# Optimization experiments

Hardware: AMD Instinct MI355X
Metric: run time of the kernel (lower is better)

## Reference

```python
import jax, jax.numpy as jnp
import numpy as np

N_NODES = 100000


def _gcn_conv(x, w, b, edge_index, n):
    # Linear transform
    x = x @ w + b
    # Add self loops
    loops = jnp.tile(jnp.arange(n, dtype=edge_index.dtype), (2, 1))
    ei = jnp.concatenate([edge_index, loops], axis=1)
    src, tgt = ei[0], ei[1]
    # Degree of source nodes (every node has a self loop -> deg >= 1)
    deg = jax.ops.segment_sum(jnp.ones(src.shape, x.dtype), src, num_segments=n)
    dinv = deg ** -0.5
    norm = dinv[src] * dinv[tgt]  # [E+N]
    # Gather-scale-scatter: out[t] += norm_e * x[s]
    msgs = norm[:, None] * x[src]  # [E+N, out_ch]
    return jax.ops.segment_sum(msgs, tgt, num_segments=n)


def setup_inputs() -> dict:
    key = jax.random.key(0)
    ks = jax.random.split(key, 6)
    n, f_in, hid, n_cls, e = N_NODES, 512, 16, 40, 3200000
    x = jax.random.normal(ks[0], (n, f_in), dtype=jnp.float32)
    edge_index = jax.random.randint(ks[1], (2, e), 0, n, dtype=jnp.int64)
    w1 = jax.random.normal(ks[2], (f_in, hid), dtype=jnp.float32) * (1.0 / np.sqrt(f_in))
    b1 = jax.random.normal(ks[3], (hid,), dtype=jnp.float32) * 0.01
    w2 = jax.random.normal(ks[4], (hid, n_cls), dtype=jnp.float32) * (1.0 / np.sqrt(hid))
    b2 = jax.random.normal(ks[5], (n_cls,), dtype=jnp.float32) * 0.01
    return {"x": x, "edge_index": edge_index, "w1": w1, "b1": b1, "w2": w2, "b2": b2}


def reference(x, edge_index, w1, b1, w2, b2):
    n = x.shape[0]
    h = _gcn_conv(x, w1, b1, edge_index, n)
    h = jax.nn.relu(h)
    # dropout is identity in eval mode (F.dropout with training=False)
    h = _gcn_conv(h, w2, b2, edge_index, n)
    return jax.nn.log_softmax(h, axis=1)
```

## Files before the change

### kernel.cpp

```cpp
#include <hip/hip_runtime.h>
#include <hip/hip_fp16.h>
#include <cstdint>

#define FIN 512
#define HID 16
#define NCLS 40
#define SHIFT 8
#define NBCAP 512
#define NBLK 512
#define BR 64
#define KC 32

typedef int   iv4 __attribute__((ext_vector_type(4)));
typedef float fv4 __attribute__((ext_vector_type(4)));


__global__ void count_kernel(const int* __restrict__ ei, int E, int nb,
                             int* __restrict__ hist_src_g, int* __restrict__ hist_tgt_g) {
    __shared__ int hs[NBCAP], ht[NBCAP];
    for (int j = threadIdx.x; j < NBCAP; j += 256) { hs[j] = 0; ht[j] = 0; }
    __syncthreads();
    if ((E & 3) == 0) {
        const iv4* s4 = (const iv4*)ei;
        const iv4* t4 = (const iv4*)(ei + E);
        int E4 = E >> 2;
        for (int i = blockIdx.x * 256 + threadIdx.x; i < E4; i += NBLK * 256) {
            iv4 s = __builtin_nontemporal_load(&s4[i]);
            iv4 t = __builtin_nontemporal_load(&t4[i]);
            atomicAdd(&hs[s.x >> SHIFT], 1); atomicAdd(&hs[s.y >> SHIFT], 1);
            atomicAdd(&hs[s.z >> SHIFT], 1); atomicAdd(&hs[s.w >> SHIFT], 1);
            atomicAdd(&ht[t.x >> SHIFT], 1); atomicAdd(&ht[t.y >> SHIFT], 1);
            atomicAdd(&ht[t.z >> SHIFT], 1); atomicAdd(&ht[t.w >> SHIFT], 1);
        }
    } else {
        for (int i = blockIdx.x * 256 + threadIdx.x; i < E; i += NBLK * 256) {
            atomicAdd(&hs[ei[i] >> SHIFT], 1);
            atomicAdd(&ht[ei[E + i] >> SHIFT], 1);
        }
    }
    __syncthreads();
    int base = blockIdx.x * NBCAP;
    for (int j = threadIdx.x; j < NBCAP; j += 256) {
        hist_src_g[base + j] = hs[j];
        hist_tgt_g[base + j] = ht[j];
    }
}


__global__ void colscan_kernel(int* __restrict__ hist_src_g, int* __restrict__ hist_tgt_g,
                               int* __restrict__ btot) {
    __shared__ int tmp[NBLK];
    int b = blockIdx.x;
    int* h = blockIdx.y ? hist_tgt_g : hist_src_g;
    int t = threadIdx.x;
    int v = h[t * NBCAP + b];
    tmp[t] = v;
    __syncthreads();
    for (int off = 1; off < NBLK; off <<= 1) {
        int a = (t >= off) ? tmp[t - off] : 0;
        __syncthreads();
        tmp[t] += a;
        __syncthreads();
    }
    h[t * NBCAP + b] = tmp[t] - v;
    if (t == NBLK - 1) btot[blockIdx.y * NBCAP + b] = tmp[NBLK - 1];
}


__global__ void bucketscan_kernel(const int* __restrict__ btot, int nb,
                                  int* __restrict__ src_base, int* __restrict__ tgt_base,
                                  int* __restrict__ row_ptr, int N, int E) {
    __shared__ int tmp[512];
    int t = threadIdx.x;
    int v = (t < nb) ? btot[t] : 0;
    tmp[t] = v;
    __syncthreads();
    for (int off = 1; off < 512; off <<= 1) {
        int a = (t >= off) ? tmp[t - off] : 0;
        __syncthreads();
        tmp[t] += a;
        __syncthreads();
    }
    if (t < nb) src_base[t] = tmp[t] - v;
    __syncthreads();
    int v2 = (t < nb) ? btot[NBCAP + t] : 0;
    tmp[t] = v2;
    __syncthreads();
    for (int off = 1; off < 512; off <<= 1) {
        int a = (t >= off) ? tmp[t - off] : 0;
        __syncthreads();
        tmp[t] += a;
        __syncthreads();
    }
    if (t < nb) tgt_base[t] = tmp[t] - v2;
    if (t == 0) { src_base[nb] = E; tgt_base[nb] = E; row_ptr[N] = E; }
}


__global__ void scatter_kernel(const int* __restrict__ ei, int E, int nb,
                               const int* __restrict__ hist_src_g,
                               const int* __restrict__ hist_tgt_g,
                               const int* __restrict__ src_base,
                               const int* __restrict__ tgt_base,
                               unsigned char* __restrict__ tmp_src,
                               unsigned int* __restrict__ tmp_tgt) {
    __shared__ int cs[NBCAP], ct[NBCAP];
    int blk = blockIdx.x;
    for (int j = threadIdx.x; j < nb; j += 256) {
        cs[j] = src_base[j] + hist_src_g[blk * NBCAP + j];
        ct[j] = tgt_base[j] + hist_tgt_g[blk * NBCAP + j];
    }
    __syncthreads();
    if ((E & 3) == 0) {
        const iv4* s4 = (const iv4*)ei;
        const iv4* t4 = (const iv4*)(ei + E);
        int E4 = E >> 2;
        for (int i = blk * 256 + threadIdx.x; i < E4; i += NBLK * 256) {
            iv4 s = __builtin_nontemporal_load(&s4[i]);
            iv4 t = __builtin_nontemporal_load(&t4[i]);
            int p;
            p = atomicAdd(&cs[s.x >> SHIFT], 1); tmp_src[p] = (unsigned char)(s.x & 255);
            p = atomicAdd(&cs[s.y >> SHIFT], 1); tmp_src[p] = (unsigned char)(s.y & 255);
            p = atomicAdd(&cs[s.z >> SHIFT], 1); tmp_src[p] = (unsigned char)(s.z & 255);
            p = atomicAdd(&cs[s.w >> SHIFT], 1); tmp_src[p] = (unsigned char)(s.w & 255);
            p = atomicAdd(&ct[t.x >> SHIFT], 1); tmp_tgt[p] = ((unsigned int)(t.x & 255) << 17) | (unsigned int)s.x;
            p = atomicAdd(&ct[t.y >> SHIFT], 1); tmp_tgt[p] = ((unsigned int)(t.y & 255) << 17) | (unsigned int)s.y;
            p = atomicAdd(&ct[t.z >> SHIFT], 1); tmp_tgt[p] = ((unsigned int)(t.z & 255) << 17) | (unsigned int)s.z;
            p = atomicAdd(&ct[t.w >> SHIFT], 1); tmp_tgt[p] = ((unsigned int)(t.w & 255) << 17) | (unsigned int)s.w;
        }
    } else {
        for (int i = blk * 256 + threadIdx.x; i < E; i += NBLK * 256) {
            int s = ei[i], tg = ei[E + i];
            int ps = atomicAdd(&cs[s >> SHIFT], 1);
            tmp_src[ps] = (unsigned char)(s & 255);
            int pt = atomicAdd(&ct[tg >> SHIFT], 1);
            tmp_tgt[pt] = ((unsigned int)(tg & 255) << 17) | (unsigned int)s;
        }
    }
}


__global__ void fine_kernel(const unsigned char* __restrict__ tmp_src,
                            const int* __restrict__ src_base,
                            const unsigned int* __restrict__ tmp_tgt,
                            const int* __restrict__ tgt_base,
                            float* __restrict__ dinv, int* __restrict__ row_ptr,
                            int* __restrict__ edges, int N) {
    __shared__ int hist[256];
    __shared__ int scan[256];
    int b = blockIdx.x;
    int t = threadIdx.x;
    hist[t] = 0;
    __syncthreads();
    {
        int beg = src_base[b], end = src_base[b + 1];
        for (int i = beg + t; i < end; i += 256)
            atomicAdd(&hist[tmp_src[i]], 1);
    }
    __syncthreads();
    int node = b * 256 + t;
    if (node < N) dinv[node] = rsqrtf((float)(hist[t] + 1));
    __syncthreads();
    hist[t] = 0;
    __syncthreads();
    int beg = tgt_base[b], end = tgt_base[b + 1];
    for (int i = beg + t; i < end; i += 256)
        atomicAdd(&hist[tmp_tgt[i] >> 17], 1);
    __syncthreads();
    int v = hist[t];
    scan[t] = v;
    __syncthreads();
    for (int off = 1; off < 256; off <<= 1) {
        int a = (t >= off) ? scan[t - off] : 0;
        __syncthreads();
        scan[t] += a;
        __syncthreads();
    }
    int ex = scan[t] - v;
    if (node < N) row_ptr[node] = beg + ex;
    hist[t] = ex;
    __syncthreads();
    for (int i = beg + t; i < end; i += 256) {
        unsigned int w = tmp_tgt[i];
        int tl = (int)(w >> 17);
        int src = (int)(w & 0x1FFFF);
        int pos = beg + atomicAdd(&hist[tl], 1);
        edges[pos] = src;
    }
}


__global__ __launch_bounds__(256, 4)
void linear1_kernel(const float* __restrict__ x, const float* __restrict__ w1,
                    const float* __restrict__ b1, __half* __restrict__ h1h, int n) {
    __shared__ float xs[KC][BR + 2];
    __shared__ float wsc[KC * HID];
    __shared__ float bl[HID];
    int t = threadIdx.x;
    if (t < HID) bl[t] = b1[t];
    int row0 = blockIdx.x * BR;
    int rp = t >> 2;
    int cq = (t & 3) * 4;
    float acc[4] = {0, 0, 0, 0};

    fv4 xp[2];
    float wp[2];
    int rr_[2], kk_[2];
#pragma unroll
    for (int u = 0; u < 2; ++u) {
        int i = t + u * 256;
        rr_[u] = i >> 3;
        kk_[u] = (i & 7) * 4;
    }
    auto prefetch = [&](int kc) {
#pragma unroll
        for (int u = 0; u < 2; ++u) {
            int grow = row0 + rr_[u];
            if (grow < n) {
                xp[u] = __builtin_nontemporal_load((const fv4*)(x + (size_t)grow * FIN + kc + kk_[u]));
            } else {
                xp[u] = (fv4){0.f, 0.f, 0.f, 0.f};
            }
        }
        wp[0] = w1[kc * HID + t];
        wp[1] = w1[kc * HID + t + 256];
    };

    prefetch(0);
    for (int kc = 0; kc < FIN; kc += KC) {
        __syncthreads();
#pragma unroll
        for (int u = 0; u < 2; ++u) {
            xs[kk_[u] + 0][rr_[u]] = xp[u].x;
            xs[kk_[u] + 1][rr_[u]] = xp[u].y;
            xs[kk_[u] + 2][rr_[u]] = xp[u].z;
            xs[kk_[u] + 3][rr_[u]] = xp[u].w;
        }
        wsc[t] = wp[0];
        wsc[t + 256] = wp[1];
        __syncthreads();
        if (kc + KC < FIN) prefetch(kc + KC);
#pragma unroll 8
        for (int k = 0; k < KC; ++k) {
            float xv = xs[k][rp];
            float4 wv = *(const float4*)&wsc[k * HID + cq];
            acc[0] = fmaf(xv, wv.x, acc[0]);
            acc[1] = fmaf(xv, wv.y, acc[1]);
            acc[2] = fmaf(xv, wv.z, acc[2]);
            acc[3] = fmaf(xv, wv.w, acc[3]);
        }
    }
    int r0 = row0 + rp;
    if (r0 < n) {
        __half2* hp = (__half2*)(h1h + (size_t)r0 * HID + cq);
        hp[0] = __floats2half2_rn(acc[0] + bl[cq + 0], acc[1] + bl[cq + 1]);
        hp[1] = __floats2half2_rn(acc[2] + bl[cq + 2], acc[3] + bl[cq + 3]);
    }
}


__global__ void agg1_kernel(const __half* __restrict__ in, const int* __restrict__ edges,
                            const int* __restrict__ row_ptr, const float* __restrict__ dinv,
                            __half* __restrict__ out16, float* __restrict__ rowsum, int n) {
    int gid = blockIdx.x * blockDim.x + threadIdx.x;
    int node = gid >> 5;
    int sub = (gid >> 3) & 3;
    int c2 = gid & 7;
    if (node >= n) return;
    const __half2* tab = (const __half2*)in;
    float dv = dinv[node];
    float a0 = 0.f, a1 = 0.f, rs = 0.f;
    if (sub == 0) {
        float self = dv * dv;
        float2 sv = __half22float2(tab[(size_t)node * 8 + c2]);
        a0 = self * sv.x; a1 = self * sv.y; rs = self;
    }
    int beg = row_ptr[node], end = row_ptr[node + 1];
#pragma unroll 4
    for (int i = beg + sub; i < end; i += 4) {
        int src = edges[i];
        float nrm = dinv[src] * dv;
        float2 v = __half22float2(tab[(size_t)src * 8 + c2]);
        a0 = fmaf(nrm, v.x, a0);
        a1 = fmaf(nrm, v.y, a1);
        rs += nrm;
    }
    a0 += __shfl_xor(a0, 8);  a1 += __shfl_xor(a1, 8);  rs += __shfl_xor(rs, 8);
    a0 += __shfl_xor(a0, 16); a1 += __shfl_xor(a1, 16); rs += __shfl_xor(rs, 16);
    if (sub == 0) {
        a0 = fmaxf(a0, 0.f); a1 = fmaxf(a1, 0.f);
        ((__half2*)out16)[(size_t)node * 8 + c2] = __floats2half2_rn(a0, a1);
        if (c2 == 0) rowsum[node] = rs;
    }
}


__global__ void agg2_kernel(const __half* __restrict__ in, const int* __restrict__ edges,
                            const int* __restrict__ row_ptr, const float* __restrict__ dinv,
                            const float* __restrict__ rowsum,
                            const float* __restrict__ w2, const float* __restrict__ b2,
                            float* __restrict__ out, int n) {
    __shared__ float g2[8][HID + 1];
    __shared__ float wl[HID * NCLS];
    __shared__ float bl[NCLS];
    int t = threadIdx.x;
    for (int i = t; i < HID * NCLS; i += 256) wl[i] = w2[i];
    if (t < NCLS) bl[t] = b2[t];
    int gid = blockIdx.x * 256 + t;
    int node = gid >> 5;
    int sub = (t >> 3) & 3;
    int c2 = t & 7;
    int nl = t >> 5;
    float a0 = 0.f, a1 = 0.f;
    if (node < n) {
        const __half2* tab = (const __half2*)in;
        float dv = dinv[node];
        if (sub == 0) {
            float self = dv * dv;
            float2 sv = __half22float2(tab[(size_t)node * 8 + c2]);
            a0 = self * sv.x; a1 = self * sv.y;
        }
        int beg = row_ptr[node], end = row_ptr[node + 1];
#pragma unroll 4
        for (int i = beg + sub; i < end; i += 4) {
            int src = edges[i];
            float nrm = dinv[src] * dv;
            float2 v = __half22float2(tab[(size_t)src * 8 + c2]);
            a0 = fmaf(nrm, v.x, a0);
            a1 = fmaf(nrm, v.y, a1);
        }
    }
    a0 += __shfl_xor(a0, 8);  a1 += __shfl_xor(a1, 8);
    a0 += __shfl_xor(a0, 16); a1 += __shfl_xor(a1, 16);
    if (sub == 0) { g2[nl][c2 * 2] = a0; g2[nl][c2 * 2 + 1] = a1; }
    __syncthreads();
    if (t < 16) {
        int nl2 = t >> 1, half = t & 1;
        int node2 = blockIdx.x * 8 + nl2;
        float z[20];
        float m = -1e30f, se = 0.f;
        if (node2 < n) {
            float h[HID];
#pragma unroll
            for (int j = 0; j < HID; ++j) h[j] = g2[nl2][j];
            float rs = rowsum[node2];
            int c0 = half * 20;
#pragma unroll
            for (int c = 0; c < 20; ++c) {
                float s = rs * bl[c0 + c];
#pragma unroll
                for (int j = 0; j < HID; ++j) s = fmaf(h[j], wl[j * NCLS + c0 + c], s);
                z[c] = s;
            }
            m = z[0];
#pragma unroll
            for (int c = 1; c < 20; ++c) m = fmaxf(m, z[c]);
        }
        m = fmaxf(m, __shfl_xor(m, 1));
        if (node2 < n) {
#pragma unroll
            for (int c = 0; c < 20; ++c) se += __expf(z[c] - m);
        }
        se += __shfl_xor(se, 1);
        if (node2 < n) {
            float lse = m + __logf(se);
            float* orow = out + (size_t)node2 * NCLS + half * 20;
#pragma unroll
            for (int c = 0; c < 20; ++c) orow[c] = z[c] - lse;
        }
    }
}


extern "C" void kernel_launch(void* const* d_in, const int* in_sizes, int n_in,
                              void* d_out, int out_size, void* d_ws, size_t ws_size,
                              hipStream_t stream) {
    const float* x  = (const float*)d_in[0];
    const int*   ei = (const int*)d_in[1];
    const float* w1 = (const float*)d_in[2];
    const float* b1 = (const float*)d_in[3];
    const float* w2 = (const float*)d_in[4];
    const float* b2 = (const float*)d_in[5];
    float* out = (float*)d_out;

    int N = in_sizes[0] / FIN;
    int E = in_sizes[1] / 2;
    int nb = (N + 255) >> SHIFT;

    char* p = (char*)d_ws;
    auto alloc = [&](size_t bytes) -> char* {
        char* r = p;
        p += (bytes + 255) / 256 * 256;
        return r;
    };
    int*   hist_src_g = (int*)alloc((size_t)NBLK * NBCAP * 4);
    int*   hist_tgt_g = (int*)alloc((size_t)NBLK * NBCAP * 4);
    int*   btot       = (int*)alloc((size_t)2 * NBCAP * 4);
    int*   src_base   = (int*)alloc((size_t)(nb + 1) * 4);
    int*   tgt_base   = (int*)alloc((size_t)(nb + 1) * 4);
    float* dinv       = (float*)alloc((size_t)N * 4);
    int*   row_ptr    = (int*)alloc((size_t)(N + 1) * 4);
    unsigned char* tmp_src = (unsigned char*)alloc((size_t)E);
    unsigned int*  tmp_tgt = (unsigned int*)alloc((size_t)E * 4);
    int*    edges     = (int*)alloc((size_t)E * 4);
    __half* h1h       = (__half*)alloc((size_t)N * HID * 2);
    __half* gh        = (__half*)alloc((size_t)N * HID * 2);
    float*  rowsum    = (float*)alloc((size_t)N * 4);

    count_kernel<<<NBLK, 256, 0, stream>>>(ei, E, nb, hist_src_g, hist_tgt_g);
    colscan_kernel<<<dim3(nb, 2), NBLK, 0, stream>>>(hist_src_g, hist_tgt_g, btot);
    bucketscan_kernel<<<1, 512, 0, stream>>>(btot, nb, src_base, tgt_base, row_ptr, N, E);
    scatter_kernel<<<NBLK, 256, 0, stream>>>(ei, E, nb, hist_src_g, hist_tgt_g,
                                             src_base, tgt_base, tmp_src, tmp_tgt);
    fine_kernel<<<nb, 256, 0, stream>>>(tmp_src, src_base, tmp_tgt, tgt_base,
                                        dinv, row_ptr, edges, N);
    linear1_kernel<<<(N + BR - 1) / BR, 256, 0, stream>>>(x, w1, b1, h1h, N);
    agg1_kernel<<<(N * 32 + 255) / 256, 256, 0, stream>>>(h1h, edges, row_ptr, dinv,
                                                          gh, rowsum, N);
    agg2_kernel<<<(N * 32 + 255) / 256, 256, 0, stream>>>(gh, edges, row_ptr, dinv,
                                                          rowsum, w2, b2, out, N);
}
```

Baseline: 516.0 us.

## Compute degrees with global atomics and fold source normalisation into linear1

Source degrees are now counted with global atomics into a per-node array. This replaces the source-side bucket sort, which needed a second histogram, a second column scan, the tmp_src scatter and a fine pass. dinv is computed inside the scatter kernel, and fine_kernel stages each target bucket in LDS so tmp_tgt is read from global memory only once. The dinv[src] factor is pre-applied to the linear1 output, and dinv[tgt] is applied once after the reduction, so the agg2 inner loop drops its per-edge dinv gather and multiply. The trade-offs are about 3.2M contended global atomics, an extra zeroing kernel, and a 48KB LDS buffer that may reduce occupancy in fine_kernel.

```diff
diff --git a/kernel.cpp b/kernel.cpp
--- a/kernel.cpp
+++ b/kernel.cpp
@@ -10,15 +10,22 @@
 #define NBLK 512
 #define BR 64
 #define KC 32
+#define FCAP 12288
 
 typedef int   iv4 __attribute__((ext_vector_type(4)));
 typedef float fv4 __attribute__((ext_vector_type(4)));
 
 
-__global__ void count_kernel(const int* __restrict__ ei, int E, int nb,
-                             int* __restrict__ hist_src_g, int* __restrict__ hist_tgt_g) {
-    __shared__ int hs[NBCAP], ht[NBCAP];
-    for (int j = threadIdx.x; j < NBCAP; j += 256) { hs[j] = 0; ht[j] = 0; }
+__global__ void zero_kernel(int* __restrict__ deg, int n) {
+    int i = blockIdx.x * 256 + threadIdx.x;
+    if (i < n) deg[i] = 0;
+}
+
+
+__global__ void count_kernel(const int* __restrict__ ei, int E,
+                             int* __restrict__ hist_tgt_g, int* __restrict__ deg) {
+    __shared__ int ht[NBCAP];
+    for (int j = threadIdx.x; j < NBCAP; j += 256) ht[j] = 0;
     __syncthreads();
     if ((E & 3) == 0) {
         const iv4* s4 = (const iv4*)ei;
@@ -27,33 +34,28 @@
         for (int i = blockIdx.x * 256 + threadIdx.x; i < E4; i += NBLK * 256) {
             iv4 s = __builtin_nontemporal_load(&s4[i]);
             iv4 t = __builtin_nontemporal_load(&t4[i]);
-            atomicAdd(&hs[s.x >> SHIFT], 1); atomicAdd(&hs[s.y >> SHIFT], 1);
-            atomicAdd(&hs[s.z >> SHIFT], 1); atomicAdd(&hs[s.w >> SHIFT], 1);
+            atomicAdd(&deg[s.x], 1); atomicAdd(&deg[s.y], 1);
+            atomicAdd(&deg[s.z], 1); atomicAdd(&deg[s.w], 1);
             atomicAdd(&ht[t.x >> SHIFT], 1); atomicAdd(&ht[t.y >> SHIFT], 1);
             atomicAdd(&ht[t.z >> SHIFT], 1); atomicAdd(&ht[t.w >> SHIFT], 1);
         }
     } else {
         for (int i = blockIdx.x * 256 + threadIdx.x; i < E; i += NBLK * 256) {
-            atomicAdd(&hs[ei[i] >> SHIFT], 1);
+            atomicAdd(&deg[ei[i]], 1);
             atomicAdd(&ht[ei[E + i] >> SHIFT], 1);
         }
     }
     __syncthreads();
     int base = blockIdx.x * NBCAP;
-    for (int j = threadIdx.x; j < NBCAP; j += 256) {
-        hist_src_g[base + j] = hs[j];
-        hist_tgt_g[base + j] = ht[j];
-    }
-}
-
-
-__global__ void colscan_kernel(int* __restrict__ hist_src_g, int* __restrict__ hist_tgt_g,
-                               int* __restrict__ btot) {
+    for (int j = threadIdx.x; j < NBCAP; j += 256) hist_tgt_g[base + j] = ht[j];
+}
+
+
+__global__ void colscan_kernel(int* __restrict__ hist_tgt_g, int* __restrict__ btot) {
     __shared__ int tmp[NBLK];
     int b = blockIdx.x;
-    int* h = blockIdx.y ? hist_tgt_g : hist_src_g;
     int t = threadIdx.x;
-    int v = h[t * NBCAP + b];
+    int v = hist_tgt_g[t * NBCAP + b];
     tmp[t] = v;
     __syncthreads();
     for (int off = 1; off < NBLK; off <<= 1) {
@@ -62,13 +64,13 @@
         tmp[t] += a;
         __syncthreads();
     }
-    h[t * NBCAP + b] = tmp[t] - v;
-    if (t == NBLK - 1) btot[blockIdx.y * NBCAP + b] = tmp[NBLK - 1];
+    hist_tgt_g[t * NBCAP + b] = tmp[t] - v;
+    if (t == NBLK - 1) btot[b] = tmp[NBLK - 1];
 }
 
 
 __global__ void bucketscan_kernel(const int* __restrict__ btot, int nb,
-                                  int* __restrict__ src_base, int* __restrict__ tgt_base,
+                                  int* __restrict__ tgt_base,
                                   int* __restrict__ row_ptr, int N, int E) {
     __shared__ int tmp[512];
     int t = threadIdx.x;
@@ -81,35 +83,23 @@
         tmp[t] += a;
         __syncthreads();
     }
-    if (t < nb) src_base[t] = tmp[t] - v;
-    __syncthreads();
-    int v2 = (t < nb) ? btot[NBCAP + t] : 0;
-    tmp[t] = v2;
-    __syncthreads();
-    for (int off = 1; off < 512; off <<= 1) {
-        int a = (t >= off) ? tmp[t - off] : 0;
-        __syncthreads();
-        tmp[t] += a;
-        __syncthreads();
-    }
-    if (t < nb) tgt_base[t] = tmp[t] - v2;
-    if (t == 0) { src_base[nb] = E; tgt_base[nb] = E; row_ptr[N] = E; }
+    if (t < nb) tgt_base[t] = tmp[t] - v;
+    if (t == 0) { tgt_base[nb] = E; row_ptr[N] = E; }
 }
 
 
 __global__ void scatter_kernel(const int* __restrict__ ei, int E, int nb,
-                               const int* __restrict__ hist_src_g,
                                const int* __restrict__ hist_tgt_g,
-                               const int* __restrict__ src_base,
                                const int* __restrict__ tgt_base,
-                               unsigned char* __restrict__ tmp_src,
-                               unsigned int* __restrict__ tmp_tgt) {
-    __shared__ int cs[NBCAP], ct[NBCAP];
+                               const int* __restrict__ deg,
+                               float* __restrict__ dinv,
+                               unsigned int* __restrict__ tmp_tgt, int N) {
+    __shared__ int ct[NBCAP];
     int blk = blockIdx.x;
-    for (int j = threadIdx.x; j < nb; j += 256) {
-        cs[j] = src_base[j] + hist_src_g[blk * NBCAP + j];
+    int i0 = blk * 256 + threadIdx.x;
+    if (i0 < N) dinv[i0] = rsqrtf((float)(deg[i0] + 1));
+    for (int j = threadIdx.x; j < nb; j += 256)
         ct[j] = tgt_base[j] + hist_tgt_g[blk * NBCAP + j];
-    }
     __syncthreads();
     if ((E & 3) == 0) {
         const iv4* s4 = (const iv4*)ei;
@@ -119,10 +109,6 @@
             iv4 s = __builtin_nontemporal_load(&s4[i]);
             iv4 t = __builtin_nontemporal_load(&t4[i]);
             int p;
-            p = atomicAdd(&cs[s.x >> SHIFT], 1); tmp_src[p] = (unsigned char)(s.x & 255);
-            p = atomicAdd(&cs[s.y >> SHIFT], 1); tmp_src[p] = (unsigned char)(s.y & 255);
-            p = atomicAdd(&cs[s.z >> SHIFT], 1); tmp_src[p] = (unsigned char)(s.z & 255);
-            p = atomicAdd(&cs[s.w >> SHIFT], 1); tmp_src[p] = (unsigned char)(s.w & 255);
             p = atomicAdd(&ct[t.x >> SHIFT], 1); tmp_tgt[p] = ((unsigned int)(t.x & 255) << 17) | (unsigned int)s.x;
             p = atomicAdd(&ct[t.y >> SHIFT], 1); tmp_tgt[p] = ((unsigned int)(t.y & 255) << 17) | (unsigned int)s.y;
             p = atomicAdd(&ct[t.z >> SHIFT], 1); tmp_tgt[p] = ((unsigned int)(t.z & 255) << 17) | (unsigned int)s.z;
@@ -131,8 +117,6 @@
     } else {
         for (int i = blk * 256 + threadIdx.x; i < E; i += NBLK * 256) {
             int s = ei[i], tg = ei[E + i];
-            int ps = atomicAdd(&cs[s >> SHIFT], 1);
-            tmp_src[ps] = (unsigned char)(s & 255);
             int pt = atomicAdd(&ct[tg >> SHIFT], 1);
             tmp_tgt[pt] = ((unsigned int)(tg & 255) << 17) | (unsigned int)s;
         }
@@ -140,32 +124,26 @@
 }
 
 
-__global__ void fine_kernel(const unsigned char* __restrict__ tmp_src,
-                            const int* __restrict__ src_base,
-                            const unsigned int* __restrict__ tmp_tgt,
+__global__ void fine_kernel(const unsigned int* __restrict__ tmp_tgt,
                             const int* __restrict__ tgt_base,
-                            float* __restrict__ dinv, int* __restrict__ row_ptr,
-                            int* __restrict__ edges, int N) {
+                            int* __restrict__ row_ptr, int* __restrict__ edges, int N) {
+    __shared__ unsigned int stage[FCAP];
     __shared__ int hist[256];
     __shared__ int scan[256];
     int b = blockIdx.x;
     int t = threadIdx.x;
+    int beg = tgt_base[b], end = tgt_base[b + 1];
+    int cnt = end - beg;
+    bool staged = (cnt <= FCAP);
     hist[t] = 0;
-    __syncthreads();
-    {
-        int beg = src_base[b], end = src_base[b + 1];
-        for (int i = beg + t; i < end; i += 256)
-            atomicAdd(&hist[tmp_src[i]], 1);
-    }
-    __syncthreads();
-    int node = b * 256 + t;
-    if (node < N) dinv[node] = rsqrtf((float)(hist[t] + 1));
-    __syncthreads();
-    hist[t] = 0;
-    __syncthreads();
-    int beg = tgt_base[b], end = tgt_base[b + 1];
-    for (int i = beg + t; i < end; i += 256)
-        atomicAdd(&hist[tmp_tgt[i] >> 17], 1);
+    if (staged)
+        for (int i = t; i < cnt; i += 256) stage[i] = tmp_tgt[beg + i];
+    __syncthreads();
+    if (staged) {
+        for (int i = t; i < cnt; i += 256) atomicAdd(&hist[stage[i] >> 17], 1);
+    } else {
+        for (int i = t; i < cnt; i += 256) atomicAdd(&hist[tmp_tgt[beg + i] >> 17], 1);
+    }
     __syncthreads();
     int v = hist[t];
     scan[t] = v;
@@ -177,22 +155,30 @@
         __syncthreads();
     }
     int ex = scan[t] - v;
+    int node = b * 256 + t;
     if (node < N) row_ptr[node] = beg + ex;
     hist[t] = ex;
     __syncthreads();
-    for (int i = beg + t; i < end; i += 256) {
-        unsigned int w = tmp_tgt[i];
-        int tl = (int)(w >> 17);
-        int src = (int)(w & 0x1FFFF);
-        int pos = beg + atomicAdd(&hist[tl], 1);
-        edges[pos] = src;
+    if (staged) {
+        for (int i = t; i < cnt; i += 256) {
+            unsigned int w = stage[i];
+            int tl = (int)(w >> 17);
+            edges[beg + atomicAdd(&hist[tl], 1)] = (int)(w & 0x1FFFF);
+        }
+    } else {
+        for (int i = t; i < cnt; i += 256) {
+            unsigned int w = tmp_tgt[beg + i];
+            int tl = (int)(w >> 17);
+            edges[beg + atomicAdd(&hist[tl], 1)] = (int)(w & 0x1FFFF);
+        }
     }
 }
 
 
 __global__ __launch_bounds__(256, 4)
 void linear1_kernel(const float* __restrict__ x, const float* __restrict__ w1,
-                    const float* __restrict__ b1, __half* __restrict__ h1h, int n) {
+                    const float* __restrict__ b1, const float* __restrict__ dinv,
+                    __half* __restrict__ h1h, int n) {
     __shared__ float xs[KC][BR + 2];
     __shared__ float wsc[KC * HID];
     __shared__ float bl[HID];
@@ -252,9 +238,10 @@
     }
     int r0 = row0 + rp;
     if (r0 < n) {
+        float dv = dinv[r0];
         __half2* hp = (__half2*)(h1h + (size_t)r0 * HID + cq);
-        hp[0] = __floats2half2_rn(acc[0] + bl[cq + 0], acc[1] + bl[cq + 1]);
-        hp[1] = __floats2half2_rn(acc[2] + bl[cq + 2], acc[3] + bl[cq + 3]);
+        hp[0] = __floats2half2_rn(dv * (acc[0] + bl[cq + 0]), dv * (acc[1] + bl[cq + 1]));
+        hp[1] = __floats2half2_rn(dv * (acc[2] + bl[cq + 2]), dv * (acc[3] + bl[cq + 3]));
     }
 }
 
@@ -271,26 +258,26 @@
     float dv = dinv[node];
     float a0 = 0.f, a1 = 0.f, rs = 0.f;
     if (sub == 0) {
-        float self = dv * dv;
         float2 sv = __half22float2(tab[(size_t)node * 8 + c2]);
-        a0 = self * sv.x; a1 = self * sv.y; rs = self;
+        a0 = sv.x; a1 = sv.y; rs = dv;
     }
     int beg = row_ptr[node], end = row_ptr[node + 1];
 #pragma unroll 4
     for (int i = beg + sub; i < end; i += 4) {
         int src = edges[i];
-        float nrm = dinv[src] * dv;
         float2 v = __half22float2(tab[(size_t)src * 8 + c2]);
-        a0 = fmaf(nrm, v.x, a0);
-        a1 = fmaf(nrm, v.y, a1);
-        rs += nrm;
+        a0 += v.x;
+        a1 += v.y;
+        rs += dinv[src];
     }
     a0 += __shfl_xor(a0, 8);  a1 += __shfl_xor(a1, 8);  rs += __shfl_xor(rs, 8);
     a0 += __shfl_xor(a0, 16); a1 += __shfl_xor(a1, 16); rs += __shfl_xor(rs, 16);
     if (sub == 0) {
-        a0 = fmaxf(a0, 0.f); a1 = fmaxf(a1, 0.f);
+        float dv2 = dv * dv;
+        a0 = fmaxf(dv2 * a0, 0.f);
+        a1 = fmaxf(dv2 * a1, 0.f);
         ((__half2*)out16)[(size_t)node * 8 + c2] = __floats2half2_rn(a0, a1);
-        if (c2 == 0) rowsum[node] = rs;
+        if (c2 == 0) rowsum[node] = dv * rs;
     }
 }
 
@@ -312,27 +299,26 @@
     int c2 = t & 7;
     int nl = t >> 5;
     float a0 = 0.f, a1 = 0.f;
+    float dv = 0.f;
     if (node < n) {
         const __half2* tab = (const __half2*)in;
-        float dv = dinv[node];
+        dv = dinv[node];
         if (sub == 0) {
-            float self = dv * dv;
             float2 sv = __half22float2(tab[(size_t)node * 8 + c2]);
-            a0 = self * sv.x; a1 = self * sv.y;
+            a0 = sv.x; a1 = sv.y;
         }
         int beg = row_ptr[node], end = row_ptr[node + 1];
 #pragma unroll 4
         for (int i = beg + sub; i < end; i += 4) {
             int src = edges[i];
-            float nrm = dinv[src] * dv;
             float2 v = __half22float2(tab[(size_t)src * 8 + c2]);
-            a0 = fmaf(nrm, v.x, a0);
-            a1 = fmaf(nrm, v.y, a1);
+            a0 += v.x;
+            a1 += v.y;
         }
     }
     a0 += __shfl_xor(a0, 8);  a1 += __shfl_xor(a1, 8);
     a0 += __shfl_xor(a0, 16); a1 += __shfl_xor(a1, 16);
-    if (sub == 0) { g2[nl][c2 * 2] = a0; g2[nl][c2 * 2 + 1] = a1; }
+    if (sub == 0) { g2[nl][c2 * 2] = dv * a0; g2[nl][c2 * 2 + 1] = dv * a1; }
     __syncthreads();
     if (t < 16) {
         int nl2 = t >> 1, half = t & 1;
@@ -393,28 +379,26 @@
         p += (bytes + 255) / 256 * 256;
         return r;
     };
-    int*   hist_src_g = (int*)alloc((size_t)NBLK * NBCAP * 4);
     int*   hist_tgt_g = (int*)alloc((size_t)NBLK * NBCAP * 4);
-    int*   btot       = (int*)alloc((size_t)2 * NBCAP * 4);
-    int*   src_base   = (int*)alloc((size_t)(nb + 1) * 4);
+    int*   btot       = (int*)alloc((size_t)NBCAP * 4);
     int*   tgt_base   = (int*)alloc((size_t)(nb + 1) * 4);
+    int*   deg        = (int*)alloc((size_t)N * 4);
     float* dinv       = (float*)alloc((size_t)N * 4);
     int*   row_ptr    = (int*)alloc((size_t)(N + 1) * 4);
-    unsigned char* tmp_src = (unsigned char*)alloc((size_t)E);
-    unsigned int*  tmp_tgt = (unsigned int*)alloc((size_t)E * 4);
+    unsigned int* tmp_tgt = (unsigned int*)alloc((size_t)E * 4);
     int*    edges     = (int*)alloc((size_t)E * 4);
     __half* h1h       = (__half*)alloc((size_t)N * HID * 2);
     __half* gh        = (__half*)alloc((size_t)N * HID * 2);
     float*  rowsum    = (float*)alloc((size_t)N * 4);
 
-    count_kernel<<<NBLK, 256, 0, stream>>>(ei, E, nb, hist_src_g, hist_tgt_g);
-    colscan_kernel<<<dim3(nb, 2), NBLK, 0, stream>>>(hist_src_g, hist_tgt_g, btot);
-    bucketscan_kernel<<<1, 512, 0, stream>>>(btot, nb, src_base, tgt_base, row_ptr, N, E);
-    scatter_kernel<<<NBLK, 256, 0, stream>>>(ei, E, nb, hist_src_g, hist_tgt_g,
-                                             src_base, tgt_base, tmp_src, tmp_tgt);
-    fine_kernel<<<nb, 256, 0, stream>>>(tmp_src, src_base, tmp_tgt, tgt_base,
-                                        dinv, row_ptr, edges, N);
-    linear1_kernel<<<(N + BR - 1) / BR, 256, 0, stream>>>(x, w1, b1, h1h, N);
+    zero_kernel<<<(N + 255) / 256, 256, 0, stream>>>(deg, N);
+    count_kernel<<<NBLK, 256, 0, stream>>>(ei, E, hist_tgt_g, deg);
+    colscan_kernel<<<nb, NBLK, 0, stream>>>(hist_tgt_g, btot);
+    bucketscan_kernel<<<1, 512, 0, stream>>>(btot, nb, tgt_base, row_ptr, N, E);
+    scatter_kernel<<<NBLK, 256, 0, stream>>>(ei, E, nb, hist_tgt_g, tgt_base,
+                                             deg, dinv, tmp_tgt, N);
+    fine_kernel<<<nb, 256, 0, stream>>>(tmp_tgt, tgt_base, row_ptr, edges, N);
+    linear1_kernel<<<(N + BR - 1) / BR, 256, 0, stream>>>(x, w1, b1, dinv, h1h, N);
     agg1_kernel<<<(N * 32 + 255) / 256, 256, 0, stream>>>(h1h, edges, row_ptr, dinv,
                                                           gh, rowsum, N);
     agg2_kernel<<<(N * 32 + 255) / 256, 256, 0, stream>>>(gh, edges, row_ptr, dinv,
```

New measurement: 592.6 us. 1.15x slower.

## Pre-scale features by inverse degree and stage target buckets in LDS

Applied to the files above, without the earlier changes.

The symmetric normalisation is factored so that linear1 multiplies each row by its own dinv. The aggregation kernels then sum neighbour features unweighted and apply the target-side dinv once per node, which drops the per-edge dinv[src] gather and multiply in agg2 and the per-edge multiplies in agg1. Separately, fine_kernel copies its target-bucket entries into a 48 KB shared buffer once and reuses them for the histogram and the placement pass, removing a second global read of tmp_tgt. The large shared allocation may lower occupancy of fine_kernel, and the reordered scaling slightly changes fp16 rounding.

```diff
diff --git a/kernel.cpp b/kernel.cpp
--- a/kernel.cpp
+++ b/kernel.cpp
@@ -10,12 +10,13 @@
 #define NBLK 512
 #define BR 64
 #define KC 32
+#define FCAP 12288
 
 typedef int   iv4 __attribute__((ext_vector_type(4)));
 typedef float fv4 __attribute__((ext_vector_type(4)));
 
 
-__global__ void count_kernel(const int* __restrict__ ei, int E, int nb,
+__global__ void count_kernel(const int* __restrict__ ei, int E,
                              int* __restrict__ hist_src_g, int* __restrict__ hist_tgt_g) {
     __shared__ int hs[NBCAP], ht[NBCAP];
     for (int j = threadIdx.x; j < NBCAP; j += 256) { hs[j] = 0; ht[j] = 0; }
@@ -146,28 +147,33 @@
                             const int* __restrict__ tgt_base,
                             float* __restrict__ dinv, int* __restrict__ row_ptr,
                             int* __restrict__ edges, int N) {
+    __shared__ unsigned int stage[FCAP];
     __shared__ int hist[256];
+    __shared__ int h2[256];
     __shared__ int scan[256];
     int b = blockIdx.x;
     int t = threadIdx.x;
+    int sb = src_base[b], se = src_base[b + 1];
+    int beg = tgt_base[b], end = tgt_base[b + 1];
+    int cnt = end - beg;
+    bool staged = (cnt <= FCAP);
     hist[t] = 0;
-    __syncthreads();
-    {
-        int beg = src_base[b], end = src_base[b + 1];
-        for (int i = beg + t; i < end; i += 256)
-            atomicAdd(&hist[tmp_src[i]], 1);
-    }
+    h2[t] = 0;
+    __syncthreads();
+    if (staged)
+        for (int i = t; i < cnt; i += 256) stage[i] = tmp_tgt[beg + i];
+    for (int i = sb + t; i < se; i += 256)
+        atomicAdd(&hist[tmp_src[i]], 1);
     __syncthreads();
     int node = b * 256 + t;
     if (node < N) dinv[node] = rsqrtf((float)(hist[t] + 1));
-    __syncthreads();
-    hist[t] = 0;
-    __syncthreads();
-    int beg = tgt_base[b], end = tgt_base[b + 1];
-    for (int i = beg + t; i < end; i += 256)
-        atomicAdd(&hist[tmp_tgt[i] >> 17], 1);
-    __syncthreads();
-    int v = hist[t];
+    if (staged) {
+        for (int i = t; i < cnt; i += 256) atomicAdd(&h2[stage[i] >> 17], 1);
+    } else {
+        for (int i = t; i < cnt; i += 256) atomicAdd(&h2[tmp_tgt[beg + i] >> 17], 1);
+    }
+    __syncthreads();
+    int v = h2[t];
     scan[t] = v;
     __syncthreads();
     for (int off = 1; off < 256; off <<= 1) {
@@ -178,21 +184,28 @@
     }
     int ex = scan[t] - v;
     if (node < N) row_ptr[node] = beg + ex;
-    hist[t] = ex;
-    __syncthreads();
-    for (int i = beg + t; i < end; i += 256) {
-        unsigned int w = tmp_tgt[i];
-        int tl = (int)(w >> 17);
-        int src = (int)(w & 0x1FFFF);
-        int pos = beg + atomicAdd(&hist[tl], 1);
-        edges[pos] = src;
+    h2[t] = ex;
+    __syncthreads();
+    if (staged) {
+        for (int i = t; i < cnt; i += 256) {
+            unsigned int w = stage[i];
+            int tl = (int)(w >> 17);
+            edges[beg + atomicAdd(&h2[tl], 1)] = (int)(w & 0x1FFFF);
+        }
+    } else {
+        for (int i = t; i < cnt; i += 256) {
+            unsigned int w = tmp_tgt[beg + i];
+            int tl = (int)(w >> 17);
+            edges[beg + atomicAdd(&h2[tl], 1)] = (int)(w & 0x1FFFF);
+        }
     }
 }
 
 
 __global__ __launch_bounds__(256, 4)
 void linear1_kernel(const float* __restrict__ x, const float* __restrict__ w1,
-                    const float* __restrict__ b1, __half* __restrict__ h1h, int n) {
+                    const float* __restrict__ b1, const float* __restrict__ dinv,
+                    __half* __restrict__ h1h, int n) {
     __shared__ float xs[KC][BR + 2];
     __shared__ float wsc[KC * HID];
     __shared__ float bl[HID];
@@ -252,9 +265,10 @@
     }
     int r0 = row0 + rp;
     if (r0 < n) {
+        float dv = dinv[r0];
         __half2* hp = (__half2*)(h1h + (size_t)r0 * HID + cq);
-        hp[0] = __floats2half2_rn(acc[0] + bl[cq + 0], acc[1] + bl[cq + 1]);
-        hp[1] = __floats2half2_rn(acc[2] + bl[cq + 2], acc[3] + bl[cq + 3]);
+        hp[0] = __floats2half2_rn(dv * (acc[0] + bl[cq + 0]), dv * (acc[1] + bl[cq + 1]));
+        hp[1] = __floats2half2_rn(dv * (acc[2] + bl[cq + 2]), dv * (acc[3] + bl[cq + 3]));
     }
 }
 
@@ -271,26 +285,26 @@
     float dv = dinv[node];
     float a0 = 0.f, a1 = 0.f, rs = 0.f;
     if (sub == 0) {
-        float self = dv * dv;
         float2 sv = __half22float2(tab[(size_t)node * 8 + c2]);
-        a0 = self * sv.x; a1 = self * sv.y; rs = self;
+        a0 = sv.x; a1 = sv.y; rs = dv;
     }
     int beg = row_ptr[node], end = row_ptr[node + 1];
 #pragma unroll 4
     for (int i = beg + sub; i < end; i += 4) {
         int src = edges[i];
-        float nrm = dinv[src] * dv;
         float2 v = __half22float2(tab[(size_t)src * 8 + c2]);
-        a0 = fmaf(nrm, v.x, a0);
-        a1 = fmaf(nrm, v.y, a1);
-        rs += nrm;
+        a0 += v.x;
+        a1 += v.y;
+        rs += dinv[src];
     }
     a0 += __shfl_xor(a0, 8);  a1 += __shfl_xor(a1, 8);  rs += __shfl_xor(rs, 8);
     a0 += __shfl_xor(a0, 16); a1 += __shfl_xor(a1, 16); rs += __shfl_xor(rs, 16);
     if (sub == 0) {
-        a0 = fmaxf(a0, 0.f); a1 = fmaxf(a1, 0.f);
+        float dv2 = dv * dv;
+        a0 = fmaxf(dv2 * a0, 0.f);
+        a1 = fmaxf(dv2 * a1, 0.f);
         ((__half2*)out16)[(size_t)node * 8 + c2] = __floats2half2_rn(a0, a1);
-        if (c2 == 0) rowsum[node] = rs;
+        if (c2 == 0) rowsum[node] = dv * rs;
     }
 }
 
@@ -312,27 +326,26 @@
     int c2 = t & 7;
     int nl = t >> 5;
     float a0 = 0.f, a1 = 0.f;
+    float dv = 0.f;
     if (node < n) {
         const __half2* tab = (const __half2*)in;
-        float dv = dinv[node];
+        dv = dinv[node];
         if (sub == 0) {
-            float self = dv * dv;
             float2 sv = __half22float2(tab[(size_t)node * 8 + c2]);
-            a0 = self * sv.x; a1 = self * sv.y;
+            a0 = sv.x; a1 = sv.y;
         }
         int beg = row_ptr[node], end = row_ptr[node + 1];
 #pragma unroll 4
         for (int i = beg + sub; i < end; i += 4) {
             int src = edges[i];
-            float nrm = dinv[src] * dv;
             float2 v = __half22float2(tab[(size_t)src * 8 + c2]);
-            a0 = fmaf(nrm, v.x, a0);
-            a1 = fmaf(nrm, v.y, a1);
+            a0 += v.x;
+            a1 += v.y;
         }
     }
     a0 += __shfl_xor(a0, 8);  a1 += __shfl_xor(a1, 8);
     a0 += __shfl_xor(a0, 16); a1 += __shfl_xor(a1, 16);
-    if (sub == 0) { g2[nl][c2 * 2] = a0; g2[nl][c2 * 2 + 1] = a1; }
+    if (sub == 0) { g2[nl][c2 * 2] = dv * a0; g2[nl][c2 * 2 + 1] = dv * a1; }
     __syncthreads();
     if (t < 16) {
         int nl2 = t >> 1, half = t & 1;
@@ -407,14 +420,14 @@
     __half* gh        = (__half*)alloc((size_t)N * HID * 2);
     float*  rowsum    = (float*)alloc((size_t)N * 4);
 
-    count_kernel<<<NBLK, 256, 0, stream>>>(ei, E, nb, hist_src_g, hist_tgt_g);
+    count_kernel<<<NBLK, 256, 0, stream>>>(ei, E, hist_src_g, hist_tgt_g);
     colscan_kernel<<<dim3(nb, 2), NBLK, 0, stream>>>(hist_src_g, hist_tgt_g, btot);
     bucketscan_kernel<<<1, 512, 0, stream>>>(btot, nb, src_base, tgt_base, row_ptr, N, E);
     scatter_kernel<<<NBLK, 256, 0, stream>>>(ei, E, nb, hist_src_g, hist_tgt_g,
                                              src_base, tgt_base, tmp_src, tmp_tgt);
     fine_kernel<<<nb, 256, 0, stream>>>(tmp_src, src_base, tmp_tgt, tgt_base,
                                         dinv, row_ptr, edges, N);
-    linear1_kernel<<<(N + BR - 1) / BR, 256, 0, stream>>>(x, w1, b1, h1h, N);
+    linear1_kernel<<<(N + BR - 1) / BR, 256, 0, stream>>>(x, w1, b1, dinv, h1h, N);
     agg1_kernel<<<(N * 32 + 255) / 256, 256, 0, stream>>>(h1h, edges, row_ptr, dinv,
                                                           gh, rowsum, N);
     agg2_kernel<<<(N * 32 + 255) / 256, 256, 0, stream>>>(gh, edges, row_ptr, dinv,
```

Result: faster. 503.5 us (-2.4%).
